# Optimization experiments

Measured on AMD Instinct MI355X. Metric: run time of the kernel, lower is better.

The kernel has to match this reference:

```python
import jax, jax.numpy as jnp
import numpy as np

NEG_SLOPE = 0.2  # PyG GATConv default leaky_relu slope
BN_EPS = 1e-5


def gat_conv(x, src, dst, num_nodes, W, a_src, a_dst, bias, concat):
    """PyG-style GATConv (eval mode, self-loops already appended to src/dst)."""
    H, F = a_src.shape
    h = (x @ W).reshape(num_nodes, H, F)              # [N,H,F]
    e_src = jnp.einsum('nhf,hf->nh', h, a_src)        # [N,H]
    e_dst = jnp.einsum('nhf,hf->nh', h, a_dst)        # [N,H]
    e = jax.nn.leaky_relu(e_src[src] + e_dst[dst], NEG_SLOPE)  # [E,H]
    m = jax.ops.segment_max(e, dst, num_segments=num_nodes)    # segment softmax (stable)
    w = jnp.exp(e - m[dst])
    z = jax.ops.segment_sum(w, dst, num_segments=num_nodes)
    alpha = w / (z[dst] + 1e-16)                      # [E,H]
    msg = alpha[:, :, None] * h[src]                  # [E,H,F]
    out = jax.ops.segment_sum(msg, dst, num_segments=num_nodes)  # [N,H,F]
    out = out.reshape(num_nodes, H * F) if concat else out.mean(axis=1)
    return out + bias


def bn_eval(x, gamma, beta):
    # BatchNorm1d eval with initialized running stats (mean=0, var=1)
    return x * (gamma / jnp.sqrt(1.0 + BN_EPS)) + beta


def setup_inputs() -> dict:
    key = jax.random.key(0)
    ks = jax.random.split(key, 16)
    N, E, Fin, H, Fh, MLP = 50000, 800000, 128, 4, 32, 64
    HF = H * Fh  # 128
    s = 0.05
    inp = {
        'x': jax.random.normal(ks[0], (N, Fin), jnp.float32),
        'edge_index': jax.random.randint(ks[1], (2, E), 0, N, jnp.int64),
        # conv0: Fin -> Fh per head, concat
        'W1': jax.random.normal(ks[2], (Fin, HF), jnp.float32) * s,
        'a1s': jax.random.normal(ks[3], (H, Fh), jnp.float32) * s,
        'a1d': jax.random.normal(ks[4], (H, Fh), jnp.float32) * s,
        'b1': jnp.zeros((HF,), jnp.float32),
        # conv1: HF -> Fh per head, concat
        'W2': jax.random.normal(ks[5], (HF, HF), jnp.float32) * s,
        'a2s': jax.random.normal(ks[6], (H, Fh), jnp.float32) * s,
        'a2d': jax.random.normal(ks[7], (H, Fh), jnp.float32) * s,
        'b2': jnp.zeros((HF,), jnp.float32),
        # mlp block 0
        'M1w': jax.random.normal(ks[8], (HF, MLP), jnp.float32) * s,
        'M1b': jnp.zeros((MLP,), jnp.float32),
        'g1': jnp.ones((MLP,), jnp.float32),
        'be1': jnp.zeros((MLP,), jnp.float32),
        'M2w': jax.random.normal(ks[9], (MLP, HF), jnp.float32) * s,
        'M2b': jnp.zeros((HF,), jnp.float32),
        'g2': jnp.ones((HF,), jnp.float32),
        'be2': jnp.zeros((HF,), jnp.float32),
        # conv2: HF -> Fh per head, mean over heads (concat=False)
        'W3': jax.random.normal(ks[10], (HF, HF), jnp.float32) * s,
        'a3s': jax.random.normal(ks[11], (H, Fh), jnp.float32) * s,
        'a3d': jax.random.normal(ks[12], (H, Fh), jnp.float32) * s,
        'b3': jnp.zeros((Fh,), jnp.float32),
    }
    return inp


def reference(x, edge_index, W1, a1s, a1d, b1, W2, a2s, a2d, b2,
              M1w, M1b, g1, be1, M2w, M2b, g2, be2, W3, a3s, a3d, b3):
    N = x.shape[0]
    loops = jnp.arange(N, dtype=edge_index.dtype)
    src = jnp.concatenate([edge_index[0], loops])  # add self-loops (PyG default)
    dst = jnp.concatenate([edge_index[1], loops])

    # layer 0: conv -> relu -> (dropout=id, eval) -> mlp[0]
    h = jax.nn.relu(gat_conv(x, src, dst, N, W1, a1s, a1d, b1, concat=True))
    h = bn_eval(jax.nn.relu(h @ M1w + M1b), g1, be1)
    h = bn_eval(jax.nn.relu(h @ M2w + M2b), g2, be2)

    # layer 1: conv -> relu -> (dropout=id)
    h = jax.nn.relu(gat_conv(h, src, dst, N, W2, a2s, a2d, b2, concat=True))

    # output layer: concat=False -> mean over heads
    out = gat_conv(h, src, dst, N, W3, a3s, a3d, b3, concat=False)
    return out
```

## Files before the change

### kernel.cpp

```cpp
#include <hip/hip_runtime.h>
#include <hip/hip_bf16.h>

#define NEG_SLOPE 0.2f
#define BN_RS 0.9999950000374997f

typedef __attribute__((ext_vector_type(8))) _Float16 f16x8;
typedef __attribute__((ext_vector_type(2))) _Float16 f16x2;
typedef __attribute__((ext_vector_type(4))) float f32x4;

__device__ __forceinline__ void store_split(float w, _Float16* H, _Float16* L, size_t off) {
  _Float16 h = (_Float16)w;
  H[off] = h;
  L[off] = (_Float16)(w - (float)h);
}


__global__ void zero256(int* p) { p[threadIdx.x] = 0; }

__global__ void eb_hist(const int* __restrict__ ei, int* __restrict__ bucketSize, int E) {
  __shared__ int h[256];
  int tid = threadIdx.x;
  h[tid] = 0;
  __syncthreads();
  for (int i = blockIdx.x * 256 + tid; i < E; i += gridDim.x * 256)
    atomicAdd(&h[ei[E + i] >> 8], 1);
  __syncthreads();
  if (h[tid]) atomicAdd(&bucketSize[tid], h[tid]);
}

__global__ void eb_scan(const int* __restrict__ bucketSize, int* __restrict__ edgeStart,
                        int* __restrict__ cursor, int* __restrict__ csrStart, int N) {
  __shared__ int sd[256];
  int tid = threadIdx.x;
  int v = bucketSize[tid];
  sd[tid] = v;
  __syncthreads();
  for (int off = 1; off < 256; off <<= 1) {
    int t = (tid >= off) ? sd[tid - off] : 0;
    __syncthreads();
    sd[tid] += t;
    __syncthreads();
  }
  int excl = sd[tid] - v;
  edgeStart[tid] = excl;
  cursor[tid] = excl;
  csrStart[tid] = excl + min(tid << 8, N);
  if (tid == 255) edgeStart[256] = sd[255];
}

#define PCH 4096
__global__ __launch_bounds__(256) void eb_part(const int* __restrict__ ei,
                                               int* __restrict__ cursor,
                                               unsigned* __restrict__ staging, int E) {
  __shared__ unsigned val[PCH];
  __shared__ unsigned char bk[PCH];
  __shared__ int cnt[256];
  __shared__ int base[256];
  int tid = threadIdx.x;
  cnt[tid] = 0;
  __syncthreads();
  int e0 = blockIdx.x * PCH;
  int n = min(PCH, E - e0);
  for (int j = tid; j < n; j += 256) {
    int s = ei[e0 + j], d = ei[E + e0 + j];
    val[j] = ((unsigned)(d & 255) << 16) | (unsigned)s;
    int b = d >> 8;
    bk[j] = (unsigned char)b;
    atomicAdd(&cnt[b], 1);
  }
  __syncthreads();
  if (cnt[tid]) base[tid] = atomicAdd(&cursor[tid], cnt[tid]);
  __syncthreads();
  for (int j = tid; j < n; j += 256) {
    int b = bk[j];
    int off = atomicSub(&cnt[b], 1) - 1;
    staging[base[b] + off] = val[j];
  }
}

__global__ __launch_bounds__(256) void eb_csr(
    const unsigned* __restrict__ staging, const int* __restrict__ edgeStart,
    const int* __restrict__ csrStart, int* __restrict__ rowptr,
    int* __restrict__ csr, int N) {
  __shared__ int deg[256];
  __shared__ int sc[256];
  __shared__ int ex[256];
  int b = blockIdx.x, tid = threadIdx.x;
  int n0 = b << 8;
  int nn = min(256, N - n0);
  deg[tid] = (tid < nn) ? 1 : 0;
  __syncthreads();
  int s0 = edgeStart[b], s1 = edgeStart[b + 1];
  for (int j = s0 + tid; j < s1; j += 256)
    atomicAdd(&deg[staging[j] >> 16], 1);
  __syncthreads();
  int dv = deg[tid];
  sc[tid] = dv;
  __syncthreads();
  for (int off = 1; off < 256; off <<= 1) {
    int t = (tid >= off) ? sc[tid - off] : 0;
    __syncthreads();
    sc[tid] += t;
    __syncthreads();
  }
  int incl = sc[tid];
  int cbase = csrStart[b];
  ex[tid] = incl - dv;
  if (tid < nn) {
    rowptr[n0 + tid + 1] = cbase + incl;
    csr[cbase + incl - 1] = n0 + tid;
  }
  if (b == 0 && tid == 0) rowptr[0] = 0;
  deg[tid] = 0;
  __syncthreads();
  for (int j = s0 + tid; j < s1; j += 256) {
    unsigned v = staging[j];
    int dl = v >> 16;
    int src = v & 0xFFFF;
    int off = atomicAdd(&deg[dl], 1);
    csr[cbase + ex[dl] + off] = src;
  }
}

__device__ __forceinline__ void wprep_conv(const float* __restrict__ W,
                                           const float* __restrict__ as_,
                                           const float* __restrict__ ad_,
                                           _Float16* __restrict__ H, _Float16* __restrict__ L,
                                           int lb, int tid) {
  if (lb < 64) {
    int idx = lb * 256 + tid;
    int k = idx >> 7, p = idx & 127;
    store_split(W[k * 128 + p], H, L, (size_t)p * 128 + k);
  } else if (lb < 68) {
    int idx = (lb - 64) * 256 + tid;
    int rl = idx >> 7, k = idx & 127;
    const float* a = (rl < 4) ? as_ : ad_;
    int h = rl & 3;
    float s = 0.f;
#pragma unroll
    for (int f = 0; f < 32; f++) s += W[k * 128 + h * 32 + f] * a[h * 32 + f];
    store_split(s, H, L, (size_t)(128 + rl) * 128 + k);
  } else {
    int idx = (lb - 68) * 256 + tid;
    int rl = idx >> 7, k = idx & 127;
    H[(size_t)(136 + rl) * 128 + k] = (_Float16)0.f;
    L[(size_t)(136 + rl) * 128 + k] = (_Float16)0.f;
  }
}

__global__ void wprep_all(
    const float* __restrict__ W1, const float* __restrict__ a1s, const float* __restrict__ a1d,
    _Float16* __restrict__ W1H, _Float16* __restrict__ W1L,
    const float* __restrict__ W2, const float* __restrict__ a2s, const float* __restrict__ a2d,
    _Float16* __restrict__ W2H, _Float16* __restrict__ W2L,
    const float* __restrict__ W3, const float* __restrict__ a3s, const float* __restrict__ a3d,
    _Float16* __restrict__ W3H, _Float16* __restrict__ W3L,
    const float* __restrict__ M1, _Float16* __restrict__ M1H, _Float16* __restrict__ M1L,
    const float* __restrict__ M2, _Float16* __restrict__ M2H, _Float16* __restrict__ M2L) {
  int b = blockIdx.x, tid = threadIdx.x;
  if (b < 72)       wprep_conv(W1, a1s, a1d, W1H, W1L, b, tid);
  else if (b < 144) wprep_conv(W2, a2s, a2d, W2H, W2L, b - 72, tid);
  else if (b < 216) wprep_conv(W3, a3s, a3d, W3H, W3L, b - 144, tid);
  else if (b < 248) {
    int idx = (b - 216) * 256 + tid;
    int k = idx >> 6, p = idx & 63;
    store_split(M1[k * 64 + p], M1H, M1L, (size_t)p * 128 + k);
  } else {
    int idx = (b - 248) * 256 + tid;
    int k = idx >> 7, p = idx & 127;
    store_split(M2[k * 128 + p], M2H, M2L, (size_t)p * 64 + k);
  }
}

template <int PT, int PST, int K, int EPI, int AUG, typename TA>
__global__ __launch_bounds__(256) void gemm_f16(
    const TA* __restrict__ A, const _Float16* __restrict__ WtH,
    const _Float16* __restrict__ WtL, _Float16* __restrict__ C, int N,
    const float* __restrict__ bias, const float* __restrict__ gamma,
    const float* __restrict__ beta, float* __restrict__ esb,
    float* __restrict__ edb) {
  constexpr int NTILE = PT / 16;
  constexpr int CTB = NTILE / 4;
  constexpr int REM = NTILE % 4;
  constexpr int KT = K / 32;
  __shared__ _Float16 As[128 * 32];
  __shared__ _Float16 WsH[PT * 32];
  __shared__ _Float16 WsL[PT * 32];
  const int tid = threadIdx.x;
  const int wave = tid >> 6, lane = tid & 63;
  const int quad = lane >> 4, l16 = lane & 15;
  const int row0 = blockIdx.x * 128;
  const bool xw = (REM != 0) && (wave == 0);

  f32x4 acc[8][CTB + (REM ? 1 : 0)];
#pragma unroll
  for (int rt = 0; rt < 8; rt++)
#pragma unroll
    for (int nt = 0; nt < CTB + (REM ? 1 : 0); nt++) acc[rt][nt] = (f32x4){0.f, 0.f, 0.f, 0.f};

  for (int kc = 0; kc < KT; ++kc) {
    {
      int r = tid >> 1, part = tid & 1;
      int gr = row0 + r;
      _Float16* dst = &As[r * 32 + part * 16];
      if (gr < N) {
        const TA* src = A + (size_t)gr * K + kc * 32 + part * 16;
        if constexpr (sizeof(TA) == 4) {
          f16x8 h0, h1;
#pragma unroll
          for (int j = 0; j < 8; j++) { h0[j] = (_Float16)src[j]; h1[j] = (_Float16)src[8 + j]; }
          *(f16x8*)dst = h0; *(f16x8*)(dst + 8) = h1;
        } else {
          uint4 v0 = *(const uint4*)src;
          uint4 v1 = *(const uint4*)(src + 8);
          *(uint4*)dst = v0; *(uint4*)(dst + 8) = v1;
        }
      } else {
        *(uint4*)dst = make_uint4(0, 0, 0, 0);
        *(uint4*)(dst + 8) = make_uint4(0, 0, 0, 0);
      }
    }
    for (int idx = tid; idx < PT * 2; idx += 256) {
      int isL = idx >= PT;
      int p = isL ? idx - PT : idx;
      const _Float16* src = (isL ? WtL : WtH) + (size_t)p * K + kc * 32;
      _Float16* dst = (isL ? WsL : WsH) + p * 32;
      uint4 a0 = *(const uint4*)src;       uint4 a1 = *(const uint4*)(src + 8);
      uint4 a2 = *(const uint4*)(src + 16); uint4 a3 = *(const uint4*)(src + 24);
      *(uint4*)dst = a0; *(uint4*)(dst + 8) = a1;
      *(uint4*)(dst + 16) = a2; *(uint4*)(dst + 24) = a3;
    }
    __syncthreads();

    f16x8 bh[CTB], bl[CTB], bhE, blE;
#pragma unroll
    for (int nt = 0; nt < CTB; nt++) {
      int p = (wave * CTB + nt) * 16 + l16;
      bh[nt] = *(f16x8*)&WsH[p * 32 + quad * 8];
      bl[nt] = *(f16x8*)&WsL[p * 32 + quad * 8];
    }
    if constexpr (REM) {
      if (xw) {
        int p = 4 * CTB * 16 + l16;
        bhE = *(f16x8*)&WsH[p * 32 + quad * 8];
        blE = *(f16x8*)&WsL[p * 32 + quad * 8];
      }
    }
#pragma unroll
    for (int rt = 0; rt < 8; rt++) {
      f16x8 a = *(f16x8*)&As[(rt * 16 + l16) * 32 + quad * 8];
#pragma unroll
      for (int nt = 0; nt < CTB; nt++) {
        acc[rt][nt] = __builtin_amdgcn_mfma_f32_16x16x32_f16(a, bh[nt], acc[rt][nt], 0, 0, 0);
        acc[rt][nt] = __builtin_amdgcn_mfma_f32_16x16x32_f16(a, bl[nt], acc[rt][nt], 0, 0, 0);
      }
      if constexpr (REM) {
        if (xw) {
          acc[rt][CTB] = __builtin_amdgcn_mfma_f32_16x16x32_f16(a, bhE, acc[rt][CTB], 0, 0, 0);
          acc[rt][CTB] = __builtin_amdgcn_mfma_f32_16x16x32_f16(a, blE, acc[rt][CTB], 0, 0, 0);
        }
      }
    }
    __syncthreads();
  }

#pragma unroll
  for (int nt = 0; nt < CTB; nt++) {
    int c = (wave * CTB + nt) * 16 + l16;
    float bi = 0.f, ga = 0.f, be = 0.f;
    if constexpr (EPI == 1) { bi = bias[c]; ga = gamma[c] * BN_RS; be = beta[c]; }
#pragma unroll
    for (int rt = 0; rt < 8; rt++)
#pragma unroll
      for (int g = 0; g < 4; g++) {
        int r = row0 + rt * 16 + quad * 4 + g;
        if (r < N) {
          float v = acc[rt][nt][g];
          if constexpr (EPI == 1) { v += bi; v = v > 0.f ? v : 0.f; v = v * ga + be; }
          C[(size_t)r * PST + c] = (_Float16)v;
        }
      }
  }
  if constexpr (REM) {
    if (wave == 0 && l16 < 8) {
      float* dstb = (l16 < 4) ? esb : edb;
      int h = l16 & 3;
#pragma unroll
      for (int rt = 0; rt < 8; rt++)
#pragma unroll
        for (int g = 0; g < 4; g++) {
          int r = row0 + rt * 16 + quad * 4 + g;
          if (r < N) dstb[(size_t)r * 4 + h] = acc[rt][CTB][g];
        }
    }
  }
}

template <int MODE>
__global__ __launch_bounds__(256) void gat_agg(
    const _Float16* __restrict__ hx, const int* __restrict__ rowptr,
    const int* __restrict__ csr, const float* __restrict__ es,
    const float* __restrict__ ed, const float* __restrict__ bias,
    void* __restrict__ outp, int N) {
  int wid = (blockIdx.x * 256 + threadIdx.x) >> 6;
  if (wid >= N) return;
  int lane = threadIdx.x & 63;
  int beg = rowptr[wid], end = rowptr[wid + 1];
  int head = lane >> 4;
  float edv = ed[wid * 4 + head];
  float ax = 0.f, ay = 0.f, z = 0.f;
  int e = beg;
  for (; e + 4 <= end; e += 4) {
    int s0 = csr[e], s1 = csr[e + 1], s2 = csr[e + 2], s3 = csr[e + 3];
    float t0 = es[s0 * 4 + head], t1 = es[s1 * 4 + head];
    float t2 = es[s2 * 4 + head], t3 = es[s3 * 4 + head];
    f16x2 h0 = *(const f16x2*)(hx + (size_t)s0 * 128 + 2 * lane);
    f16x2 h1 = *(const f16x2*)(hx + (size_t)s1 * 128 + 2 * lane);
    f16x2 h2 = *(const f16x2*)(hx + (size_t)s2 * 128 + 2 * lane);
    f16x2 h3 = *(const f16x2*)(hx + (size_t)s3 * 128 + 2 * lane);
    t0 += edv; t1 += edv; t2 += edv; t3 += edv;
    t0 = t0 > 0.f ? t0 : NEG_SLOPE * t0;
    t1 = t1 > 0.f ? t1 : NEG_SLOPE * t1;
    t2 = t2 > 0.f ? t2 : NEG_SLOPE * t2;
    t3 = t3 > 0.f ? t3 : NEG_SLOPE * t3;
    float w0 = __expf(t0), w1 = __expf(t1), w2 = __expf(t2), w3 = __expf(t3);
    z += (w0 + w1) + (w2 + w3);
    ax = fmaf(w0, (float)h0[0], ax); ay = fmaf(w0, (float)h0[1], ay);
    ax = fmaf(w1, (float)h1[0], ax); ay = fmaf(w1, (float)h1[1], ay);
    ax = fmaf(w2, (float)h2[0], ax); ay = fmaf(w2, (float)h2[1], ay);
    ax = fmaf(w3, (float)h3[0], ax); ay = fmaf(w3, (float)h3[1], ay);
  }
  for (; e < end; ++e) {
    int s = csr[e];
    float t = es[s * 4 + head] + edv;
    t = t > 0.f ? t : NEG_SLOPE * t;
    float w = __expf(t);
    f16x2 hv = *(const f16x2*)(hx + (size_t)s * 128 + 2 * lane);
    ax = fmaf(w, (float)hv[0], ax);
    ay = fmaf(w, (float)hv[1], ay);
    z += w;
  }
  float inv = 1.f / (z + 1e-16f);
  float vx = ax * inv, vy = ay * inv;
  if (MODE == 0) {
    vx += bias[2 * lane]; vy += bias[2 * lane + 1];
    vx = vx > 0.f ? vx : 0.f;  vy = vy > 0.f ? vy : 0.f;
    f16x2 o; o[0] = (_Float16)vx; o[1] = (_Float16)vy;
    *(f16x2*)((_Float16*)outp + (size_t)wid * 128 + 2 * lane) = o;
  } else {
    vx += __shfl_xor(vx, 16); vx += __shfl_xor(vx, 32);
    vy += __shfl_xor(vy, 16); vy += __shfl_xor(vy, 32);
    if (lane < 16) {
      float ox = vx * 0.25f + bias[2 * lane];
      float oy = vy * 0.25f + bias[2 * lane + 1];
      *(float2*)((float*)outp + (size_t)wid * 32 + 2 * lane) = make_float2(ox, oy);
    }
  }
}

extern "C" void kernel_launch(void* const* d_in, const int* in_sizes, int n_in,
                              void* d_out, int out_size, void* d_ws, size_t ws_size,
                              hipStream_t stream) {
  const float* x   = (const float*)d_in[0];
  const int*   ei  = (const int*)d_in[1];
  const float* W1  = (const float*)d_in[2];
  const float* a1s = (const float*)d_in[3];
  const float* a1d = (const float*)d_in[4];
  const float* b1  = (const float*)d_in[5];
  const float* W2  = (const float*)d_in[6];
  const float* a2s = (const float*)d_in[7];
  const float* a2d = (const float*)d_in[8];
  const float* b2  = (const float*)d_in[9];
  const float* M1w = (const float*)d_in[10];
  const float* M1b = (const float*)d_in[11];
  const float* g1  = (const float*)d_in[12];
  const float* be1 = (const float*)d_in[13];
  const float* M2w = (const float*)d_in[14];
  const float* M2b = (const float*)d_in[15];
  const float* g2  = (const float*)d_in[16];
  const float* be2 = (const float*)d_in[17];
  const float* W3  = (const float*)d_in[18];
  const float* a3s = (const float*)d_in[19];
  const float* a3d = (const float*)d_in[20];
  const float* b3  = (const float*)d_in[21];

  const int N = in_sizes[0] / 128;
  const int E = in_sizes[1] / 2;

  char* w = (char*)d_ws;
  _Float16* bufA = (_Float16*)w; w += (size_t)N * 128 * 2;
  _Float16* bufB = (_Float16*)w; w += (size_t)N * 128 * 2;
  _Float16* bufM = (_Float16*)w; w += (size_t)N * 64 * 2;
  float* esb  = (float*)w; w += (size_t)N * 4 * 4;
  float* edb  = (float*)w; w += (size_t)N * 4 * 4;
  int* rowptr = (int*)w;   w += (size_t)(N + 1) * 4;
  int* csr    = (int*)w;   w += (size_t)(E + N) * 4;
  unsigned* staging = (unsigned*)w; w += (size_t)E * 4;
  int* bucketSize = (int*)w; w += 256 * 4;
  int* edgeStart  = (int*)w; w += 257 * 4;
  int* cursor     = (int*)w; w += 256 * 4;
  int* csrStart   = (int*)w; w += 256 * 4;
  _Float16* W1H = (_Float16*)w; w += 144 * 128 * 2;
  _Float16* W1L = (_Float16*)w; w += 144 * 128 * 2;
  _Float16* W2H = (_Float16*)w; w += 144 * 128 * 2;
  _Float16* W2L = (_Float16*)w; w += 144 * 128 * 2;
  _Float16* W3H = (_Float16*)w; w += 144 * 128 * 2;
  _Float16* W3L = (_Float16*)w; w += 144 * 128 * 2;
  _Float16* M1H = (_Float16*)w; w += 64 * 128 * 2;
  _Float16* M1L = (_Float16*)w; w += 64 * 128 * 2;
  _Float16* M2H = (_Float16*)w; w += 128 * 64 * 2;
  _Float16* M2L = (_Float16*)w; w += 128 * 64 * 2;

  const int gb = (N + 127) / 128;
  const int aggb = (N + 3) / 4;
  const int nbk = (N + 255) / 256;
  const int pbk = (E + PCH - 1) / PCH;

  wprep_all<<<280, 256, 0, stream>>>(W1, a1s, a1d, W1H, W1L,
                                     W2, a2s, a2d, W2H, W2L,
                                     W3, a3s, a3d, W3H, W3L,
                                     M1w, M1H, M1L, M2w, M2H, M2L);

  zero256<<<1, 256, 0, stream>>>(bucketSize);
  eb_hist<<<256, 256, 0, stream>>>(ei, bucketSize, E);
  eb_scan<<<1, 256, 0, stream>>>(bucketSize, edgeStart, cursor, csrStart, N);
  eb_part<<<pbk, 256, 0, stream>>>(ei, cursor, staging, E);
  eb_csr<<<nbk, 256, 0, stream>>>(staging, edgeStart, csrStart, rowptr, csr, N);

  gemm_f16<144, 128, 128, 0, 1, float><<<gb, 256, 0, stream>>>(
      x, W1H, W1L, bufA, N, nullptr, nullptr, nullptr, esb, edb);
  gat_agg<0><<<aggb, 256, 0, stream>>>(bufA, rowptr, csr, esb, edb, b1, bufB, N);
  gemm_f16<64, 64, 128, 1, 0, _Float16><<<gb, 256, 0, stream>>>(
      bufB, M1H, M1L, bufM, N, M1b, g1, be1, nullptr, nullptr);
  gemm_f16<128, 128, 64, 1, 0, _Float16><<<gb, 256, 0, stream>>>(
      bufM, M2H, M2L, bufA, N, M2b, g2, be2, nullptr, nullptr);

  gemm_f16<144, 128, 128, 0, 1, _Float16><<<gb, 256, 0, stream>>>(
      bufA, W2H, W2L, bufB, N, nullptr, nullptr, nullptr, esb, edb);
  gat_agg<0><<<aggb, 256, 0, stream>>>(bufB, rowptr, csr, esb, edb, b2, bufA, N);

  gemm_f16<144, 128, 128, 0, 1, _Float16><<<gb, 256, 0, stream>>>(
      bufA, W3H, W3L, bufB, N, nullptr, nullptr, nullptr, esb, edb);
  gat_agg<1><<<aggb, 256, 0, stream>>>(bufB, rowptr, csr, esb, edb, b3, d_out, N);
}
```

Baseline: 365.4 us.

## Precompute per-edge attention weights in a separate kernel before aggregation

Each CSR entry now packs the destination index into its upper 16 bits alongside the source. A new wq_comp kernel computes exp(leaky_relu(es[src]+ed[dst])) for every edge and head into a dense buffer before each aggregation. gat_agg then reads those weights contiguously instead of gathering es and recomputing the exponential, and its edge loop is unrolled from 4 to 8. The aim is to take the dependent es gather and the exp off the latency-bound gather loop. In exchange it adds three kernel launches and writes and re-reads roughly 13.6 MB of weights per layer.

```diff
diff --git a/kernel.cpp b/kernel.cpp
--- a/kernel.cpp
+++ b/kernel.cpp
@@ -81,7 +81,7 @@
 __global__ __launch_bounds__(256) void eb_csr(
     const unsigned* __restrict__ staging, const int* __restrict__ edgeStart,
     const int* __restrict__ csrStart, int* __restrict__ rowptr,
-    int* __restrict__ csr, int N) {
+    unsigned* __restrict__ csr, int N) {
   __shared__ int deg[256];
   __shared__ int sc[256];
   __shared__ int ex[256];
@@ -108,7 +108,8 @@
   ex[tid] = incl - dv;
   if (tid < nn) {
     rowptr[n0 + tid + 1] = cbase + incl;
-    csr[cbase + incl - 1] = n0 + tid;
+    unsigned me = (unsigned)(n0 + tid);
+    csr[cbase + incl - 1] = (me << 16) | me;
   }
   if (b == 0 && tid == 0) rowptr[0] = 0;
   deg[tid] = 0;
@@ -116,10 +117,23 @@
   for (int j = s0 + tid; j < s1; j += 256) {
     unsigned v = staging[j];
     int dl = v >> 16;
-    int src = v & 0xFFFF;
+    unsigned src = v & 0xFFFF;
     int off = atomicAdd(&deg[dl], 1);
-    csr[cbase + ex[dl] + off] = src;
-  }
+    csr[cbase + ex[dl] + off] = ((unsigned)(n0 + dl) << 16) | src;
+  }
+}
+
+__global__ __launch_bounds__(256) void wq_comp(
+    const unsigned* __restrict__ csr, const float* __restrict__ es,
+    const float* __restrict__ ed, float* __restrict__ wq, int S4) {
+  int i = blockIdx.x * 256 + threadIdx.x;
+  if (i >= S4) return;
+  int slot = i >> 2, head = i & 3;
+  unsigned v = csr[slot];
+  int s = v & 0xFFFF, d = v >> 16;
+  float t = es[s * 4 + head] + ed[d * 4 + head];
+  t = t > 0.f ? t : NEG_SLOPE * t;
+  wq[i] = __expf(t);
 }
 
 __device__ __forceinline__ void wprep_conv(const float* __restrict__ W,
@@ -299,46 +313,49 @@
 template <int MODE>
 __global__ __launch_bounds__(256) void gat_agg(
     const _Float16* __restrict__ hx, const int* __restrict__ rowptr,
-    const int* __restrict__ csr, const float* __restrict__ es,
-    const float* __restrict__ ed, const float* __restrict__ bias,
-    void* __restrict__ outp, int N) {
+    const unsigned* __restrict__ csr, const float* __restrict__ wq,
+    const float* __restrict__ bias, void* __restrict__ outp, int N) {
   int wid = (blockIdx.x * 256 + threadIdx.x) >> 6;
   if (wid >= N) return;
   int lane = threadIdx.x & 63;
+  int head = lane >> 4;
   int beg = rowptr[wid], end = rowptr[wid + 1];
-  int head = lane >> 4;
-  float edv = ed[wid * 4 + head];
   float ax = 0.f, ay = 0.f, z = 0.f;
+  const _Float16* hb = hx + 2 * lane;
+
   int e = beg;
-  for (; e + 4 <= end; e += 4) {
-    int s0 = csr[e], s1 = csr[e + 1], s2 = csr[e + 2], s3 = csr[e + 3];
-    float t0 = es[s0 * 4 + head], t1 = es[s1 * 4 + head];
-    float t2 = es[s2 * 4 + head], t3 = es[s3 * 4 + head];
-    f16x2 h0 = *(const f16x2*)(hx + (size_t)s0 * 128 + 2 * lane);
-    f16x2 h1 = *(const f16x2*)(hx + (size_t)s1 * 128 + 2 * lane);
-    f16x2 h2 = *(const f16x2*)(hx + (size_t)s2 * 128 + 2 * lane);
-    f16x2 h3 = *(const f16x2*)(hx + (size_t)s3 * 128 + 2 * lane);
-    t0 += edv; t1 += edv; t2 += edv; t3 += edv;
-    t0 = t0 > 0.f ? t0 : NEG_SLOPE * t0;
-    t1 = t1 > 0.f ? t1 : NEG_SLOPE * t1;
-    t2 = t2 > 0.f ? t2 : NEG_SLOPE * t2;
-    t3 = t3 > 0.f ? t3 : NEG_SLOPE * t3;
-    float w0 = __expf(t0), w1 = __expf(t1), w2 = __expf(t2), w3 = __expf(t3);
-    z += (w0 + w1) + (w2 + w3);
+  for (; e + 8 <= end; e += 8) {
+    unsigned v0 = csr[e], v1 = csr[e + 1], v2 = csr[e + 2], v3 = csr[e + 3];
+    unsigned v4 = csr[e + 4], v5 = csr[e + 5], v6 = csr[e + 6], v7 = csr[e + 7];
+    float w0 = wq[(e + 0) * 4 + head], w1 = wq[(e + 1) * 4 + head];
+    float w2 = wq[(e + 2) * 4 + head], w3 = wq[(e + 3) * 4 + head];
+    float w4 = wq[(e + 4) * 4 + head], w5 = wq[(e + 5) * 4 + head];
+    float w6 = wq[(e + 6) * 4 + head], w7 = wq[(e + 7) * 4 + head];
+    f16x2 h0 = *(const f16x2*)(hb + (size_t)(v0 & 0xFFFF) * 128);
+    f16x2 h1 = *(const f16x2*)(hb + (size_t)(v1 & 0xFFFF) * 128);
+    f16x2 h2 = *(const f16x2*)(hb + (size_t)(v2 & 0xFFFF) * 128);
+    f16x2 h3 = *(const f16x2*)(hb + (size_t)(v3 & 0xFFFF) * 128);
+    f16x2 h4 = *(const f16x2*)(hb + (size_t)(v4 & 0xFFFF) * 128);
+    f16x2 h5 = *(const f16x2*)(hb + (size_t)(v5 & 0xFFFF) * 128);
+    f16x2 h6 = *(const f16x2*)(hb + (size_t)(v6 & 0xFFFF) * 128);
+    f16x2 h7 = *(const f16x2*)(hb + (size_t)(v7 & 0xFFFF) * 128);
+    z += ((w0 + w1) + (w2 + w3)) + ((w4 + w5) + (w6 + w7));
     ax = fmaf(w0, (float)h0[0], ax); ay = fmaf(w0, (float)h0[1], ay);
     ax = fmaf(w1, (float)h1[0], ax); ay = fmaf(w1, (float)h1[1], ay);
     ax = fmaf(w2, (float)h2[0], ax); ay = fmaf(w2, (float)h2[1], ay);
     ax = fmaf(w3, (float)h3[0], ax); ay = fmaf(w3, (float)h3[1], ay);
+    ax = fmaf(w4, (float)h4[0], ax); ay = fmaf(w4, (float)h4[1], ay);
+    ax = fmaf(w5, (float)h5[0], ax); ay = fmaf(w5, (float)h5[1], ay);
+    ax = fmaf(w6, (float)h6[0], ax); ay = fmaf(w6, (float)h6[1], ay);
+    ax = fmaf(w7, (float)h7[0], ax); ay = fmaf(w7, (float)h7[1], ay);
   }
   for (; e < end; ++e) {
-    int s = csr[e];
-    float t = es[s * 4 + head] + edv;
-    t = t > 0.f ? t : NEG_SLOPE * t;
-    float w = __expf(t);
-    f16x2 hv = *(const f16x2*)(hx + (size_t)s * 128 + 2 * lane);
+    unsigned v = csr[e];
+    float w = wq[e * 4 + head];
+    f16x2 hv = *(const f16x2*)(hb + (size_t)(v & 0xFFFF) * 128);
+    z += w;
     ax = fmaf(w, (float)hv[0], ax);
     ay = fmaf(w, (float)hv[1], ay);
-    z += w;
   }
   float inv = 1.f / (z + 1e-16f);
   float vx = ax * inv, vy = ay * inv;
@@ -386,6 +403,7 @@
 
   const int N = in_sizes[0] / 128;
   const int E = in_sizes[1] / 2;
+  const int S = E + N;
 
   char* w = (char*)d_ws;
   _Float16* bufA = (_Float16*)w; w += (size_t)N * 128 * 2;
@@ -394,7 +412,8 @@
   float* esb  = (float*)w; w += (size_t)N * 4 * 4;
   float* edb  = (float*)w; w += (size_t)N * 4 * 4;
   int* rowptr = (int*)w;   w += (size_t)(N + 1) * 4;
-  int* csr    = (int*)w;   w += (size_t)(E + N) * 4;
+  unsigned* csr = (unsigned*)w; w += (size_t)S * 4;
+  float* wq   = (float*)w; w += (size_t)S * 4 * 4;
   unsigned* staging = (unsigned*)w; w += (size_t)E * 4;
   int* bucketSize = (int*)w; w += 256 * 4;
   int* edgeStart  = (int*)w; w += 257 * 4;
@@ -415,6 +434,7 @@
   const int aggb = (N + 3) / 4;
   const int nbk = (N + 255) / 256;
   const int pbk = (E + PCH - 1) / PCH;
+  const int wqb = (S * 4 + 255) / 256;
 
   wprep_all<<<280, 256, 0, stream>>>(W1, a1s, a1d, W1H, W1L,
                                      W2, a2s, a2d, W2H, W2L,
@@ -429,7 +449,8 @@
 
   gemm_f16<144, 128, 128, 0, 1, float><<<gb, 256, 0, stream>>>(
       x, W1H, W1L, bufA, N, nullptr, nullptr, nullptr, esb, edb);
-  gat_agg<0><<<aggb, 256, 0, stream>>>(bufA, rowptr, csr, esb, edb, b1, bufB, N);
+  wq_comp<<<wqb, 256, 0, stream>>>(csr, esb, edb, wq, S * 4);
+  gat_agg<0><<<aggb, 256, 0, stream>>>(bufA, rowptr, csr, wq, b1, bufB, N);
   gemm_f16<64, 64, 128, 1, 0, _Float16><<<gb, 256, 0, stream>>>(
       bufB, M1H, M1L, bufM, N, M1b, g1, be1, nullptr, nullptr);
   gemm_f16<128, 128, 64, 1, 0, _Float16><<<gb, 256, 0, stream>>>(
@@ -437,9 +458,11 @@
 
   gemm_f16<144, 128, 128, 0, 1, _Float16><<<gb, 256, 0, stream>>>(
       bufA, W2H, W2L, bufB, N, nullptr, nullptr, nullptr, esb, edb);
-  gat_agg<0><<<aggb, 256, 0, stream>>>(bufB, rowptr, csr, esb, edb, b2, bufA, N);
+  wq_comp<<<wqb, 256, 0, stream>>>(csr, esb, edb, wq, S * 4);
+  gat_agg<0><<<aggb, 256, 0, stream>>>(bufB, rowptr, csr, wq, b2, bufA, N);
 
   gemm_f16<144, 128, 128, 0, 1, _Float16><<<gb, 256, 0, stream>>>(
       bufA, W3H, W3L, bufB, N, nullptr, nullptr, nullptr, esb, edb);
-  gat_agg<1><<<aggb, 256, 0, stream>>>(bufB, rowptr, csr, esb, edb, b3, d_out, N);
-}
+  wq_comp<<<wqb, 256, 0, stream>>>(csr, esb, edb, wq, S * 4);
+  gat_agg<1><<<aggb, 256, 0, stream>>>(bufB, rowptr, csr, wq, b3, d_out, N);
+}
```

New measurement: 382.9 us. 1.05x slower.
